# Kernel tuning notes

Measured on AMD Instinct MI355X. Metric: run time of the kernel, lower is better.

Reference implementation:

```python
import jax, jax.numpy as jnp
import numpy as np
from jax import lax

FILTER = [1, 3, 3, 1]
FILTER_RADIUS = len(FILTER) // 2  # 2


def _lowpass_kernel():
    # Inplace=True branch: kernel = outer product of the raw filter, normalized.
    k = np.array([FILTER], dtype=np.float64)  # (1, 4)
    k = k.T @ k                               # (4, 4)
    return (k / k.sum()).astype(np.float32)


def _pixel_shuffle(x, scale):
    N, C, H, W = x.shape
    x = x.reshape(N, C // scale ** 2, scale, scale, H, W)
    x = jnp.transpose(x, (0, 1, 4, 2, 5, 3))
    return x.reshape(N, C // scale ** 2, H * scale, W * scale)


def setup_inputs() -> dict:
    key = jax.random.key(0)
    x = jax.random.normal(key, (32, 256, 64, 64), dtype=jnp.float32)
    return {"x": x}


def reference(x) -> jnp.ndarray:
    x = _pixel_shuffle(x, 2)  # (N, C/4, 2H, 2W)
    N, C, H, W = x.shape
    kernel = jnp.asarray(_lowpass_kernel(), dtype=x.dtype).reshape(1, 1, 4, 4)
    r = FILTER_RADIUS
    # Depthwise blur expressed as a batch-of-single-channel 2D conv (upfirdn2d style).
    y = lax.conv_general_dilated(
        x.reshape(N * C, 1, H, W),
        kernel,
        window_strides=(1, 1),
        padding=((r, r), (r, r)),
        dimension_numbers=("NCHW", "OIHW", "NCHW"),
    )
    return y.reshape(N, C, y.shape[2], y.shape[3])  # (32, 64, 129, 129)
```

## Files before the change

kernel.cpp:

```cpp
#include <hip/hip_runtime.h>


constexpr int ROWS = 33;
constexpr int HR   = 19;
constexpr int HC   = 132;

__global__ __launch_bounds__(256) void upsample_blur(
    const float* __restrict__ x, float* __restrict__ y)
{
    const int chunk = blockIdx.x;
    const int cp    = blockIdx.y;
    const int n     = blockIdx.z;
    const int tid   = threadIdx.x;

    __shared__ float h[2][HR][HC];

    const int oh0 = chunk * ROWS;
    const int m0  = oh0 >> 1;

    const float* xb = x + ((size_t)(n * 64 + cp) * 4) * 4096;

    for (int idx = tid; idx < 2 * HR * 33; idx += 256) {
        const int t  = idx % 33;
        const int rr = (idx / 33) % HR;
        const int sh = idx / (33 * HR);
        const int r  = m0 - 1 + rr;
        float h0 = 0.f, h1 = 0.f, h2 = 0.f, h3 = 0.f;
        if (r >= 0 && r < 64) {
            const float* X0 = xb + (sh * 2 + 0) * 4096 + r * 64;
            const float* X1 = xb + (sh * 2 + 1) * 4096 + r * 64;
            const int j = 2 * t;
            const float am1 = (j - 1 >= 0) ? X0[j - 1] : 0.f;
            const float a0  = (j     < 64) ? X0[j]     : 0.f;
            const float a1  = (j + 1 < 64) ? X0[j + 1] : 0.f;
            const float a2  = (j + 2 < 64) ? X0[j + 2] : 0.f;
            const float bm1 = (j - 1 >= 0) ? X1[j - 1] : 0.f;
            const float b0  = (j     < 64) ? X1[j]     : 0.f;
            const float b1  = (j + 1 < 64) ? X1[j + 1] : 0.f;
            h0 = (am1 + 3.f * a0 + 3.f * bm1 + b0) * 0.125f;
            h1 = (3.f * a0 + a1 + bm1 + 3.f * b0) * 0.125f;
            h2 = (a0 + 3.f * a1 + 3.f * b0 + b1) * 0.125f;
            h3 = (3.f * a1 + a2 + b0 + 3.f * b1) * 0.125f;
        }
        *(float4*)&h[sh][rr][4 * t] = make_float4(h0, h1, h2, h3);
    }
    __syncthreads();

    for (int idx = tid; idx < ROWS * 33; idx += 256) {
        const int t  = idx % 33;
        const int R  = idx / 33;
        const int oh = oh0 + R;
        if (oh > 128) continue;
        const int m   = oh >> 1;
        const int lm  = m - m0 + 1;
        const int par = oh & 1;

        const float4 A0 = *(const float4*)&h[0][par ? lm     : lm - 1][4 * t];
        const float4 A1 = *(const float4*)&h[0][par ? lm + 1 : lm    ][4 * t];
        const float4 B0 = *(const float4*)&h[1][lm - 1][4 * t];
        const float4 B1 = *(const float4*)&h[1][lm    ][4 * t];
        const float wA0 = par ? 3.f : 1.f;
        const float wA1 = par ? 1.f : 3.f;
        const float wB0 = par ? 1.f : 3.f;
        const float wB1 = par ? 3.f : 1.f;

        const float o0 = (wA0 * A0.x + wA1 * A1.x + wB0 * B0.x + wB1 * B1.x) * 0.125f;
        const float o1 = (wA0 * A0.y + wA1 * A1.y + wB0 * B0.y + wB1 * B1.y) * 0.125f;
        const float o2 = (wA0 * A0.z + wA1 * A1.z + wB0 * B0.z + wB1 * B1.z) * 0.125f;
        const float o3 = (wA0 * A0.w + wA1 * A1.w + wB0 * B0.w + wB1 * B1.w) * 0.125f;

        float* yp = y + ((size_t)(n * 64 + cp) * 129 + oh) * 129 + 4 * t;
        const int ow = 4 * t;
        yp[0] = o0;
        if (ow + 1 < 129) yp[1] = o1;
        if (ow + 2 < 129) yp[2] = o2;
        if (ow + 3 < 129) yp[3] = o3;
    }
}

extern "C" void kernel_launch(void* const* d_in, const int* in_sizes, int n_in,
                              void* d_out, int out_size, void* d_ws, size_t ws_size,
                              hipStream_t stream) {
    const float* x = (const float*)d_in[0];
    float* yp = (float*)d_out;
    dim3 grid(4, 64, 32);
    upsample_blur<<<grid, dim3(256), 0, stream>>>(x, yp);
}
```

Baseline: 269.2 us.

## Replace shared-memory tiling with register row-streaming and wavefront shuffles

```diff
diff --git a/kernel.cpp b/kernel.cpp
--- a/kernel.cpp
+++ b/kernel.cpp
@@ -1,80 +1,83 @@
 #include <hip/hip_runtime.h>
 
-
-constexpr int ROWS = 33;
-constexpr int HR   = 19;
-constexpr int HC   = 132;
 
 __global__ __launch_bounds__(256) void upsample_blur(
     const float* __restrict__ x, float* __restrict__ y)
 {
-    const int chunk = blockIdx.x;
-    const int cp    = blockIdx.y;
-    const int n     = blockIdx.z;
-    const int tid   = threadIdx.x;
+    const int tid  = threadIdx.x;
+    const int lane = tid & 63;
+    const int s    = tid >> 6;
+    const int b    = blockIdx.x;
 
-    __shared__ float h[2][HR][HC];
+    const float* __restrict__ x00 = x + (size_t)b * 16384;
+    const float* __restrict__ x01 = x00 + 4096;
+    const float* __restrict__ x10 = x00 + 8192;
+    const float* __restrict__ x11 = x00 + 12288;
+    float* __restrict__ yb = y + (size_t)b * 16641;
 
-    const int oh0 = chunk * ROWS;
-    const int m0  = oh0 >> 1;
+    const int m0 = s << 4;
 
-    const float* xb = x + ((size_t)(n * 64 + cp) * 4) * 4096;
+    float q10, q11;
+    float p00, p01, p10, p11;
+    float c00, c01, c10, c11;
+    float n00, n01, n10, n11;
 
-    for (int idx = tid; idx < 2 * HR * 33; idx += 256) {
-        const int t  = idx % 33;
-        const int rr = (idx / 33) % HR;
-        const int sh = idx / (33 * HR);
-        const int r  = m0 - 1 + rr;
-        float h0 = 0.f, h1 = 0.f, h2 = 0.f, h3 = 0.f;
-        if (r >= 0 && r < 64) {
-            const float* X0 = xb + (sh * 2 + 0) * 4096 + r * 64;
-            const float* X1 = xb + (sh * 2 + 1) * 4096 + r * 64;
-            const int j = 2 * t;
-            const float am1 = (j - 1 >= 0) ? X0[j - 1] : 0.f;
-            const float a0  = (j     < 64) ? X0[j]     : 0.f;
-            const float a1  = (j + 1 < 64) ? X0[j + 1] : 0.f;
-            const float a2  = (j + 2 < 64) ? X0[j + 2] : 0.f;
-            const float bm1 = (j - 1 >= 0) ? X1[j - 1] : 0.f;
-            const float b0  = (j     < 64) ? X1[j]     : 0.f;
-            const float b1  = (j + 1 < 64) ? X1[j + 1] : 0.f;
-            h0 = (am1 + 3.f * a0 + 3.f * bm1 + b0) * 0.125f;
-            h1 = (3.f * a0 + a1 + bm1 + 3.f * b0) * 0.125f;
-            h2 = (a0 + 3.f * a1 + 3.f * b0 + b1) * 0.125f;
-            h3 = (3.f * a1 + a2 + b0 + 3.f * b1) * 0.125f;
+    if (s > 0) {
+        const int off2 = (m0 - 2) * 64 + lane;
+        const int off1 = (m0 - 1) * 64 + lane;
+        q10 = x10[off2]; q11 = x11[off2];
+        p00 = x00[off1]; p01 = x01[off1];
+        p10 = x10[off1]; p11 = x11[off1];
+    } else {
+        q10 = q11 = 0.f;
+        p00 = p01 = p10 = p11 = 0.f;
+    }
+    {
+        const int off0 = m0 * 64 + lane;
+        c00 = x00[off0]; c01 = x01[off0];
+        c10 = x10[off0]; c11 = x11[off0];
+    }
+
+    const int mlast = m0 + 16;
+    const int elast = (s == 3) ? 64 : (m0 + 15);
+
+    for (int i = 0; i <= 16; ++i) {
+        const int m = m0 + i;
+
+        if (m < mlast && m + 1 < 64) {
+            const int offn = (m + 1) * 64 + lane;
+            n00 = x00[offn]; n01 = x01[offn];
+            n10 = x10[offn]; n11 = x11[offn];
+        } else {
+            n00 = n01 = n10 = n11 = 0.f;
         }
-        *(float4*)&h[sh][rr][4 * t] = make_float4(h0, h1, h2, h3);
-    }
-    __syncthreads();
 
-    for (int idx = tid; idx < ROWS * 33; idx += 256) {
-        const int t  = idx % 33;
-        const int R  = idx / 33;
-        const int oh = oh0 + R;
-        if (oh > 128) continue;
-        const int m   = oh >> 1;
-        const int lm  = m - m0 + 1;
-        const int par = oh & 1;
+        if (m > m0) {
+            const float v0 = (3.f * p00 + c00 + q10 + 3.f * p10) * 0.125f;
+            const float v1 = (3.f * p01 + c01 + q11 + 3.f * p11) * 0.125f;
+            float v0m = __shfl_up(v0, 1);   if (lane == 0)  v0m = 0.f;
+            float v1m = __shfl_up(v1, 1);   if (lane == 0)  v1m = 0.f;
+            float v0p = __shfl_down(v0, 1); if (lane == 63) v0p = 0.f;
+            float* r = yb + (size_t)(2 * m - 1) * 129;
+            r[2 * lane]     = (v0m + 3.f * v0 + 3.f * v1m + v1) * 0.125f;
+            r[2 * lane + 1] = (3.f * v0 + v0p + v1m + 3.f * v1) * 0.125f;
+            if (lane == 63) r[128] = (v0 + 3.f * v1) * 0.125f;
+        }
+        if (m <= elast) {
+            const float v0 = (p00 + 3.f * c00 + 3.f * p10 + c10) * 0.125f;
+            const float v1 = (p01 + 3.f * c01 + 3.f * p11 + c11) * 0.125f;
+            float v0m = __shfl_up(v0, 1);   if (lane == 0)  v0m = 0.f;
+            float v1m = __shfl_up(v1, 1);   if (lane == 0)  v1m = 0.f;
+            float v0p = __shfl_down(v0, 1); if (lane == 63) v0p = 0.f;
+            float* r = yb + (size_t)(2 * m) * 129;
+            r[2 * lane]     = (v0m + 3.f * v0 + 3.f * v1m + v1) * 0.125f;
+            r[2 * lane + 1] = (3.f * v0 + v0p + v1m + 3.f * v1) * 0.125f;
+            if (lane == 63) r[128] = (v0 + 3.f * v1) * 0.125f;
+        }
 
-        const float4 A0 = *(const float4*)&h[0][par ? lm     : lm - 1][4 * t];
-        const float4 A1 = *(const float4*)&h[0][par ? lm + 1 : lm    ][4 * t];
-        const float4 B0 = *(const float4*)&h[1][lm - 1][4 * t];
-        const float4 B1 = *(const float4*)&h[1][lm    ][4 * t];
-        const float wA0 = par ? 3.f : 1.f;
-        const float wA1 = par ? 1.f : 3.f;
-        const float wB0 = par ? 1.f : 3.f;
-        const float wB1 = par ? 3.f : 1.f;
-
-        const float o0 = (wA0 * A0.x + wA1 * A1.x + wB0 * B0.x + wB1 * B1.x) * 0.125f;
-        const float o1 = (wA0 * A0.y + wA1 * A1.y + wB0 * B0.y + wB1 * B1.y) * 0.125f;
-        const float o2 = (wA0 * A0.z + wA1 * A1.z + wB0 * B0.z + wB1 * B1.z) * 0.125f;
-        const float o3 = (wA0 * A0.w + wA1 * A1.w + wB0 * B0.w + wB1 * B1.w) * 0.125f;
-
-        float* yp = y + ((size_t)(n * 64 + cp) * 129 + oh) * 129 + 4 * t;
-        const int ow = 4 * t;
-        yp[0] = o0;
-        if (ow + 1 < 129) yp[1] = o1;
-        if (ow + 2 < 129) yp[2] = o2;
-        if (ow + 3 < 129) yp[3] = o3;
+        q10 = p10; q11 = p11;
+        p00 = c00; p01 = c01; p10 = c10; p11 = c11;
+        c00 = n00; c01 = n01; c10 = n10; c11 = n11;
     }
 }
 
@@ -83,6 +86,5 @@
                               hipStream_t stream) {
     const float* x = (const float*)d_in[0];
     float* yp = (float*)d_out;
-    dim3 grid(4, 64, 32);
-    upsample_blur<<<grid, dim3(256), 0, stream>>>(x, yp);
+    upsample_blur<<<dim3(2048), dim3(256), 0, stream>>>(x, yp);
 }
```

Result: faster. 252.7 us (-6.1%).
